# Kernel optimization log

Hardware: AMD Instinct MI355X
Metric: run time of the kernel (lower is better)

Reference implementation:

```python
import jax, jax.numpy as jnp
import numpy as np

N_NODES = 50000
N_EDGES = 800000
IN_DIM = 128
HIDDEN_DIMS = [128, 128]
OUT_DIM = 4
NUM_GRAPHS = 128


def setup_inputs() -> dict:
    key = jax.random.key(0)
    ks = jax.random.split(key, 12)
    inp = {
        "x": jax.random.normal(ks[0], (N_NODES, IN_DIM), dtype=jnp.float32),
        "edge_index": jax.random.randint(ks[1], (2, N_EDGES), 0, N_NODES, dtype=jnp.int64),
        "edge_attr": jax.random.uniform(ks[2], (N_EDGES,), dtype=jnp.float32),
        "edge_weight": jax.random.uniform(ks[3], (N_EDGES,), dtype=jnp.float32),
        "batch": jnp.sort(jax.random.randint(ks[4], (N_NODES,), 0, NUM_GRAPHS, dtype=jnp.int64)),
    }
    # GCNConv weights (Glorot-ish scale) and biases
    d_in = IN_DIM
    for i, d_out in enumerate(HIDDEN_DIMS):
        inp[f"W{i}"] = jax.random.normal(ks[5 + i], (d_in, d_out), dtype=jnp.float32) / np.sqrt(d_in)
        inp[f"b{i}"] = jnp.zeros((d_out,), dtype=jnp.float32)
        d_in = d_out
    # classifier: Linear(d,d) -> ReLU -> Linear(d,4)
    inp["Wc1"] = jax.random.normal(ks[8], (d_in, d_in), dtype=jnp.float32) / np.sqrt(d_in)
    inp["bc1"] = jnp.zeros((d_in,), dtype=jnp.float32)
    inp["Wc2"] = jax.random.normal(ks[9], (d_in, OUT_DIM), dtype=jnp.float32) / np.sqrt(d_in)
    inp["bc2"] = jnp.zeros((OUT_DIM,), dtype=jnp.float32)
    return inp


def _gcn_conv(x, src, dst, ew, W, b):
    # PyG GCNConv with add_self_loops=True, symmetric normalization.
    n = x.shape[0]
    loop = jnp.arange(n, dtype=src.dtype)
    s = jnp.concatenate([src, loop])
    d = jnp.concatenate([dst, loop])
    w = jnp.concatenate([ew, jnp.ones((n,), dtype=ew.dtype)])
    deg = jax.ops.segment_sum(w, d, num_segments=n)
    dinv = jnp.where(deg > 0, jax.lax.rsqrt(jnp.maximum(deg, 1e-12)), 0.0)
    norm = dinv[s] * w * dinv[d]  # [E+N]
    h = x @ W                     # [N, d_out] dense GEMM
    out = jax.ops.segment_sum(h[s] * norm[:, None], d, num_segments=n)
    return out + b


def reference(x, edge_index, edge_attr, edge_weight, batch,
              W0, b0, W1, b1, Wc1, bc1, Wc2, bc2):
    # NOTE: original code passes edge_attr into GCNConv's edge_weight slot;
    # edge_weight is unused. Dropout is identity (eval mode).
    src, dst = edge_index[0], edge_index[1]
    h = x
    for W, b in ((W0, b0), (W1, b1)):
        h = _gcn_conv(h, src, dst, edge_attr, W, b)
        h = jax.nn.relu(h)
    # global mean pool over graphs
    sums = jax.ops.segment_sum(h, batch, num_segments=NUM_GRAPHS)
    cnts = jax.ops.segment_sum(jnp.ones((h.shape[0],), h.dtype), batch, num_segments=NUM_GRAPHS)
    g = sums / jnp.maximum(cnts, 1.0)[:, None]  # [G, d]
    # classifier MLP
    g = jax.nn.relu(g @ Wc1 + bc1)
    return g @ Wc2 + bc2  # [G, 4]
```

## Files before the change

kernel.cpp:

```cpp
#include <hip/hip_runtime.h>
#include <hip/hip_fp16.h>

#define N_NODES 50000
#define N_EDGES 800000
#define DIM 128
#define NUM_GRAPHS 128
#define STRIDE 64
#define PSLICE 6272

#define ATTR_SCALE 33554432.0f
#define ATTR_MASK  ((1ull << 40) - 1)

typedef _Float16 f16x8 __attribute__((ext_vector_type(8)));
typedef float f32x4 __attribute__((ext_vector_type(4)));


__device__ __forceinline__ int pidx(int d) {
    return (d & 7) * PSLICE + (d >> 3);
}


__global__ __launch_bounds__(256) void k_build(const int* __restrict__ src,
                                               const int* __restrict__ dst,
                                               const float* __restrict__ attr,
                                               const float* __restrict__ W0,
                                               const float* __restrict__ W1,
                                               unsigned long long* packed,
                                               unsigned int* __restrict__ epack,
                                               _Float16* __restrict__ Wt0,
                                               _Float16* __restrict__ Wt1,
                                               int E, int nbChunks) {
    int b = blockIdx.x;
    if (b >= nbChunks * 8) {
        int idx = (b - nbChunks * 8) * 256 + threadIdx.x;
        int m = idx >> 14;
        int rem = idx & 16383;
        int n = rem >> 7;
        int k = rem & 127;
        const float* W = m ? W1 : W0;
        _Float16* Wt = m ? Wt1 : Wt0;
        Wt[(size_t)n * 128 + k] = (_Float16)W[(size_t)k * 128 + n];
        return;
    }
    int slice = b & 7;
    int e = (b >> 3) * 256 + threadIdx.x;
    if (e >= E) return;
    int d = dst[e];
    if ((d & 7) != slice) return;
    float a = attr[e];
    unsigned long long add =
        (1ull << 40) | (unsigned long long)(unsigned int)(a * ATTR_SCALE + 0.5f);
    unsigned long long old = atomicAdd(&packed[pidx(d)], add);
    int rank = (int)(old >> 40);
    if (rank < STRIDE) {
        __half ha = __float2half_rn(a);
        unsigned short us = *reinterpret_cast<unsigned short*>(&ha);
        epack[d * STRIDE + rank] = ((unsigned int)us << 16) | (unsigned int)src[e];
    }
}


template <typename AT>
__global__ __launch_bounds__(256) void k_gemm_mfma(const AT* __restrict__ A,
                                                   const _Float16* __restrict__ Wt,
                                                   const unsigned long long* __restrict__ packed,
                                                   __half* __restrict__ H, int n) {
    int tid = threadIdx.x;
    int w = tid >> 6, lane = tid & 63;
    int n15 = lane & 15, quad = lane >> 4;
    int node = blockIdx.x * 64 + w * 16 + n15;
    int nodec = node < n ? node : n - 1;
    const AT* Arow = A + (size_t)nodec * DIM;

    f32x4 acc[8];
#pragma unroll
    for (int t = 0; t < 8; t++) acc[t] = (f32x4){0.f, 0.f, 0.f, 0.f};

#pragma unroll
    for (int c = 0; c < 4; c++) {
        f16x8 bf;
        if constexpr (__is_same(AT, float)) {
            float4 a0 = ((const float4*)Arow)[c * 8 + quad * 2];
            float4 a1 = ((const float4*)Arow)[c * 8 + quad * 2 + 1];
            bf[0] = (_Float16)a0.x; bf[1] = (_Float16)a0.y;
            bf[2] = (_Float16)a0.z; bf[3] = (_Float16)a0.w;
            bf[4] = (_Float16)a1.x; bf[5] = (_Float16)a1.y;
            bf[6] = (_Float16)a1.z; bf[7] = (_Float16)a1.w;
        } else {
            const uint2* Ab = reinterpret_cast<const uint2*>(A);
            bf = *(const f16x8*)&Ab[((size_t)c * n + nodec) * 8 + quad * 2];
        }
#pragma unroll
        for (int t = 0; t < 8; t++) {
            f16x8 af = *(const f16x8*)(Wt + (size_t)(t * 16 + n15) * 128 + c * 32 + quad * 8);
            acc[t] = __builtin_amdgcn_mfma_f32_16x16x32_f16(af, bf, acc[t], 0, 0, 0);
        }
    }

    if (node < n) {
        unsigned long long pk = packed[pidx(nodec)];
        float dv = rsqrtf(1.0f + (float)(pk & ATTR_MASK) * (1.0f / ATTR_SCALE));
        uint2* Hb = (uint2*)H;
#pragma unroll
        for (int t = 0; t < 8; t++) {
            __half2 h01 = __floats2half2_rn(acc[t][0] * dv, acc[t][1] * dv);
            __half2 h23 = __floats2half2_rn(acc[t][2] * dv, acc[t][3] * dv);
            uint2 pkd;
            pkd.x = *reinterpret_cast<unsigned int*>(&h01);
            pkd.y = *reinterpret_cast<unsigned int*>(&h23);
            int colq = quad + 4 * t;
            Hb[((size_t)(colq >> 3) * n + node) * 8 + (colq & 7)] = pkd;
        }
    }
}


__device__ __forceinline__ float2 unpack_h2(unsigned int u) {
    __half2 h = *reinterpret_cast<__half2*>(&u);
    return __half22float2(h);
}

template <bool POOL>
__global__ __launch_bounds__(256) void k_gather(const __half* __restrict__ H,
                                                const unsigned long long* __restrict__ packed,
                                                const unsigned int* __restrict__ epack,
                                                const float* __restrict__ bias,
                                                const int* __restrict__ batch,
                                                __half* __restrict__ OUT,
                                                float* gsum, float* cnt, int n) {
    int cg = blockIdx.x & 3;
    int nb = blockIdx.x >> 2;
    int tid = threadIdx.x;

    __shared__ uint2 elds[STRIDE * 32];
    __shared__ float dv_lds[32];
    __shared__ int   cr_lds[32];

    {
        int slot = tid & 31;
        int kb = tid >> 5;
        int i1 = nb * 32 + slot;
        int ic1 = (i1 < n) ? i1 : n - 1;
        unsigned long long pk = packed[pidx(ic1)];
        int ce = (i1 < n) ? (int)(pk >> 40) : 0;
        if (ce > STRIDE) ce = STRIDE;
        int cr = (ce + 7) & ~7;
        if (kb == 0) {
            cr_lds[slot] = cr;
            dv_lds[slot] = rsqrtf(1.0f + (float)(pk & ATTR_MASK) * (1.0f / ATTR_SCALE));
        }
        const unsigned int* ep = epack + ic1 * STRIDE;
        for (int k = kb; k < cr; k += 8) {
            unsigned int pe = (k < ce) ? ep[k] : 0u;
            __half_raw hr;
            hr.x = (unsigned short)(pe >> 16);
            float wv = __half2float(__half(hr));
            elds[k * 32 + slot] = make_uint2((pe & 0xffffu) * 8u, __float_as_uint(wv));
        }
    }
    __syncthreads();

    int slot = tid >> 3;
    int ln = tid & 7;
    int i = nb * 32 + slot;
    bool valid = i < n;
    int ic = valid ? i : n - 1;
    int colq = cg * 8 + ln;
    const uint2* Hp = (const uint2*)H + (size_t)cg * n * 8;

    float dv = dv_lds[slot];
    int cr = cr_lds[slot];

    uint2 selfraw = Hp[(size_t)ic * 8 + ln];
    float2 s01 = unpack_h2(selfraw.x);
    float2 s23 = unpack_h2(selfraw.y);
    float4 acc = make_float4(s01.x, s01.y, s23.x, s23.y);

    for (int j = 0; j < cr; j += 8) {
        uint2 e[8];
#pragma unroll
        for (int k = 0; k < 8; k++) e[k] = elds[(j + k) * 32 + slot];
        uint2 v[8];
#pragma unroll
        for (int k = 0; k < 8; k++) v[k] = Hp[e[k].x + ln];
#pragma unroll
        for (int k = 0; k < 8; k++) {
            float wt = __uint_as_float(e[k].y);
            float2 f01 = unpack_h2(v[k].x);
            float2 f23 = unpack_h2(v[k].y);
            acc.x += wt * f01.x;
            acc.y += wt * f01.y;
            acc.z += wt * f23.x;
            acc.w += wt * f23.y;
        }
    }

    float4 bb = ((const float4*)bias)[colq];
    acc.x = fmaxf(acc.x * dv + bb.x, 0.f);
    acc.y = fmaxf(acc.y * dv + bb.y, 0.f);
    acc.z = fmaxf(acc.z * dv + bb.z, 0.f);
    acc.w = fmaxf(acc.w * dv + bb.w, 0.f);

    if constexpr (POOL) {
        __shared__ float lpool[32 * 32];
        __shared__ int sg[32];
        __shared__ int meta[4];
        if (ln == 0) sg[slot] = valid ? batch[ic] : -1;
        __syncthreads();
        if (tid == 0) {
            int nv = n - nb * 32; if (nv > 32) nv = 32;
            int gA = sg[0];
            int gB = sg[nv - 1];
            int cA = 0, cB = 0;
            for (int k2 = 0; k2 < nv; k2++) {
                if (sg[k2] == gA) cA++;
                else if (sg[k2] == gB) cB++;
            }
            meta[0] = gA; meta[1] = gB; meta[2] = cA; meta[3] = cB;
        }
        __syncthreads();
        int gA = meta[0], gB = meta[1];
        int myg = valid ? sg[slot] : -2;

        bool inA = valid && (myg == gA);
        ((float4*)(lpool + slot * 32))[ln] =
            inA ? acc : make_float4(0.f, 0.f, 0.f, 0.f);
        __syncthreads();
        if (tid < 32) {
            float ssum = 0.f;
#pragma unroll
            for (int k2 = 0; k2 < 32; k2++) ssum += lpool[k2 * 32 + tid];
            atomicAdd(&gsum[gA * DIM + cg * 32 + tid], ssum);
        }
        if (tid == 0 && cg == 0) atomicAdd(&cnt[gA], (float)meta[2]);

        if (gB != gA) {
            __syncthreads();
            bool inB = valid && (myg == gB);
            ((float4*)(lpool + slot * 32))[ln] =
                inB ? acc : make_float4(0.f, 0.f, 0.f, 0.f);
            __syncthreads();
            if (tid < 32) {
                float ssum = 0.f;
#pragma unroll
                for (int k2 = 0; k2 < 32; k2++) ssum += lpool[k2 * 32 + tid];
                atomicAdd(&gsum[gB * DIM + cg * 32 + tid], ssum);
            }
            if (tid == 0 && cg == 0) atomicAdd(&cnt[gB], (float)meta[3]);
        }

        if (valid && myg != gA && myg != gB) {
            float* o = gsum + (size_t)myg * DIM + cg * 32 + ln * 4;
            atomicAdd(o + 0, acc.x);
            atomicAdd(o + 1, acc.y);
            atomicAdd(o + 2, acc.z);
            atomicAdd(o + 3, acc.w);
            if (ln == 0 && cg == 0) atomicAdd(&cnt[myg], 1.0f);
        }
    } else {
        if (valid) {
            __half2 p01 = __floats2half2_rn(acc.x, acc.y);
            __half2 p23 = __floats2half2_rn(acc.z, acc.w);
            uint2 o;
            o.x = *reinterpret_cast<unsigned int*>(&p01);
            o.y = *reinterpret_cast<unsigned int*>(&p23);
            ((uint2*)OUT)[((size_t)cg * n + i) * 8 + ln] = o;
        }
    }
}


__global__ __launch_bounds__(128) void k_classifier(const float* __restrict__ gsum,
                                                    const float* __restrict__ cnt,
                                                    const float* __restrict__ Wc1,
                                                    const float* __restrict__ bc1,
                                                    const float* __restrict__ Wc2,
                                                    const float* __restrict__ bc2,
                                                    float* __restrict__ out) {
    int g = blockIdx.x;
    int t = threadIdx.x;
    __shared__ float gv[128];
    __shared__ float hid[128];
    float inv = 1.0f / fmaxf(cnt[g], 1.0f);
    gv[t] = gsum[(size_t)g * DIM + t] * inv;
    __syncthreads();
    float acc = bc1[t];
    for (int k = 0; k < 128; k++) acc += gv[k] * Wc1[k * 128 + t];
    hid[t] = fmaxf(acc, 0.f);
    __syncthreads();
    if (t < 4) {
        float o = bc2[t];
        for (int k = 0; k < 128; k++) o += hid[k] * Wc2[k * 4 + t];
        out[g * 4 + t] = o;
    }
}


extern "C" void kernel_launch(void* const* d_in, const int* in_sizes, int n_in,
                              void* d_out, int out_size, void* d_ws, size_t ws_size,
                              hipStream_t stream) {
    const float* x     = (const float*)d_in[0];
    const int*   ei    = (const int*)d_in[1];
    const float* attr  = (const float*)d_in[2];
    const int*   batch = (const int*)d_in[4];
    const float* W0  = (const float*)d_in[5];
    const float* b0  = (const float*)d_in[6];
    const float* W1  = (const float*)d_in[7];
    const float* b1  = (const float*)d_in[8];
    const float* Wc1 = (const float*)d_in[9];
    const float* bc1 = (const float*)d_in[10];
    const float* Wc2 = (const float*)d_in[11];
    const float* bc2 = (const float*)d_in[12];
    float* out = (float*)d_out;

    char* ws = (char*)d_ws;
    __half*             bufH16 = (__half*)(ws + 0);
    __half*             bufA16 = (__half*)(ws + 12800000);
    unsigned int*       epack  = (unsigned int*)(ws + 25600000);
    unsigned long long* packed = (unsigned long long*)(ws + 38400000);
    float*              gsum   = (float*)(ws + 38801408);
    float*              cnt    = (float*)(ws + 38866944);
    _Float16*           Wt0    = (_Float16*)(ws + 38867456);
    _Float16*           Wt1    = (_Float16*)(ws + 38900224);

    const int* src = ei;
    const int* dst = ei + N_EDGES;

    const int NB_C = (N_EDGES + 255) / 256;
    const int NB_G = ((N_NODES + 31) / 32) * 4;
    const int NB_M = (N_NODES + 63) / 64;

    (void)hipMemsetAsync(ws + 38400000, 0, 467456, stream);

    k_build<<<NB_C * 8 + 128, 256, 0, stream>>>(src, dst, attr, W0, W1, packed,
                                                epack, Wt0, Wt1, N_EDGES, NB_C);

    k_gemm_mfma<float><<<NB_M, 256, 0, stream>>>(x, Wt0, packed, bufH16, N_NODES);
    k_gather<false><<<NB_G, 256, 0, stream>>>(bufH16, packed, epack, b0,
                                              batch, bufA16, gsum, cnt, N_NODES);

    k_gemm_mfma<_Float16><<<NB_M, 256, 0, stream>>>((const _Float16*)bufA16, Wt1,
                                                    packed, bufH16, N_NODES);
    k_gather<true><<<NB_G, 256, 0, stream>>>(bufH16, packed, epack, b1,
                                             batch, nullptr, gsum, cnt, N_NODES);

    k_classifier<<<NUM_GRAPHS, 128, 0, stream>>>(gsum, cnt, Wc1, bc1, Wc2, bc2, out);
}
```

Baseline: 257.6 us.

## Fuse first-layer GEMM into build kernel and apply source degree scaling in gather

Runs the first-layer x@W0 GEMM inside the edge-build kernel, so it no longer has to wait for the degree accumulation; each block transposes W0 into LDS itself. Because degrees are not yet known at GEMM time, the source-side dinv scaling moves into the first gather via a new dinv array produced by a small extra kernel. The goal is to remove one launch and overlap the GEMM with the atomic-heavy edge bucketing. The cost is an extra kernel, a per-edge dinv lookup in gather staging, and every GEMM block redundantly converting W0.

```diff
diff --git a/kernel.cpp b/kernel.cpp
--- a/kernel.cpp
+++ b/kernel.cpp
@@ -20,30 +20,84 @@
 }
 
 
-__global__ __launch_bounds__(256) void k_build(const int* __restrict__ src,
+__global__ __launch_bounds__(256) void k_build(const float* __restrict__ x,
+                                               const int* __restrict__ src,
                                                const int* __restrict__ dst,
                                                const float* __restrict__ attr,
                                                const float* __restrict__ W0,
                                                const float* __restrict__ W1,
                                                unsigned long long* packed,
                                                unsigned int* __restrict__ epack,
-                                               _Float16* __restrict__ Wt0,
                                                _Float16* __restrict__ Wt1,
-                                               int E, int nbChunks) {
+                                               __half* __restrict__ H,
+                                               int E, int nbChunks, int nbGemm, int n) {
+    __shared__ _Float16 WtL[128 * 40];
     int b = blockIdx.x;
-    if (b >= nbChunks * 8) {
-        int idx = (b - nbChunks * 8) * 256 + threadIdx.x;
-        int m = idx >> 14;
-        int rem = idx & 16383;
-        int n = rem >> 7;
-        int k = rem & 127;
-        const float* W = m ? W1 : W0;
-        _Float16* Wt = m ? Wt1 : Wt0;
-        Wt[(size_t)n * 128 + k] = (_Float16)W[(size_t)k * 128 + n];
+    int tid = threadIdx.x;
+
+    if (b < nbGemm) {
+        int w = tid >> 6, lane = tid & 63;
+        int n15 = lane & 15, quad = lane >> 4;
+        int node = b * 64 + w * 16 + n15;
+        int nodec = node < n ? node : n - 1;
+        const float* Arow = x + (size_t)nodec * DIM;
+
+        f32x4 acc[8];
+#pragma unroll
+        for (int t = 0; t < 8; t++) acc[t] = (f32x4){0.f, 0.f, 0.f, 0.f};
+
+        for (int c = 0; c < 4; c++) {
+            __syncthreads();
+            {
+                int sn = tid & 127, kh = tid >> 7;
+#pragma unroll
+                for (int it = 0; it < 16; it++) {
+                    int kk = kh + it * 2;
+                    WtL[sn * 40 + kk] = (_Float16)W0[(size_t)(c * 32 + kk) * 128 + sn];
+                }
+            }
+            __syncthreads();
+            f16x8 bf;
+            float4 a0 = ((const float4*)Arow)[c * 8 + quad * 2];
+            float4 a1 = ((const float4*)Arow)[c * 8 + quad * 2 + 1];
+            bf[0] = (_Float16)a0.x; bf[1] = (_Float16)a0.y;
+            bf[2] = (_Float16)a0.z; bf[3] = (_Float16)a0.w;
+            bf[4] = (_Float16)a1.x; bf[5] = (_Float16)a1.y;
+            bf[6] = (_Float16)a1.z; bf[7] = (_Float16)a1.w;
+#pragma unroll
+            for (int t = 0; t < 8; t++) {
+                f16x8 af = *(const f16x8*)(WtL + (t * 16 + n15) * 40 + quad * 8);
+                acc[t] = __builtin_amdgcn_mfma_f32_16x16x32_f16(af, bf, acc[t], 0, 0, 0);
+            }
+        }
+
+        if (node < n) {
+            uint2* Hb = (uint2*)H;
+#pragma unroll
+            for (int t = 0; t < 8; t++) {
+                __half2 h01 = __floats2half2_rn(acc[t][0], acc[t][1]);
+                __half2 h23 = __floats2half2_rn(acc[t][2], acc[t][3]);
+                uint2 pkd;
+                pkd.x = *reinterpret_cast<unsigned int*>(&h01);
+                pkd.y = *reinterpret_cast<unsigned int*>(&h23);
+                int colq = quad + 4 * t;
+                Hb[((size_t)(colq >> 3) * n + node) * 8 + (colq & 7)] = pkd;
+            }
+        }
         return;
     }
-    int slice = b & 7;
-    int e = (b >> 3) * 256 + threadIdx.x;
+
+    if (b >= nbGemm + nbChunks * 8) {
+        int idx = (b - nbGemm - nbChunks * 8) * 256 + tid;
+        int nn = idx >> 7;
+        int kk = idx & 127;
+        Wt1[(size_t)nn * 128 + kk] = (_Float16)W1[(size_t)kk * 128 + nn];
+        return;
+    }
+
+    int b2 = b - nbGemm;
+    int slice = b2 & 7;
+    int e = (b2 >> 3) * 256 + tid;
     if (e >= E) return;
     int d = dst[e];
     if ((d & 7) != slice) return;
@@ -60,6 +114,16 @@
 }
 
 
+__global__ __launch_bounds__(256) void k_dinv(const unsigned long long* __restrict__ packed,
+                                              float* __restrict__ dinv, int n) {
+    int i = blockIdx.x * 256 + threadIdx.x;
+    if (i < n) {
+        unsigned long long pk = packed[pidx(i)];
+        dinv[i] = rsqrtf(1.0f + (float)(pk & ATTR_MASK) * (1.0f / ATTR_SCALE));
+    }
+}
+
+
 template <typename AT>
 __global__ __launch_bounds__(256) void k_gemm_mfma(const AT* __restrict__ A,
                                                    const _Float16* __restrict__ Wt,
@@ -120,10 +184,11 @@
     return __half22float2(h);
 }
 
-template <bool POOL>
+template <bool POOL, bool SRCS>
 __global__ __launch_bounds__(256) void k_gather(const __half* __restrict__ H,
                                                 const unsigned long long* __restrict__ packed,
                                                 const unsigned int* __restrict__ epack,
+                                                const float* __restrict__ dinv_arr,
                                                 const float* __restrict__ bias,
                                                 const int* __restrict__ batch,
                                                 __half* __restrict__ OUT,
@@ -155,6 +220,7 @@
             __half_raw hr;
             hr.x = (unsigned short)(pe >> 16);
             float wv = __half2float(__half(hr));
+            if (SRCS) wv *= dinv_arr[pe & 0xffffu];
             elds[k * 32 + slot] = make_uint2((pe & 0xffffu) * 8u, __float_as_uint(wv));
         }
     }
@@ -175,6 +241,9 @@
     float2 s01 = unpack_h2(selfraw.x);
     float2 s23 = unpack_h2(selfraw.y);
     float4 acc = make_float4(s01.x, s01.y, s23.x, s23.y);
+    if (SRCS) {
+        acc.x *= dv; acc.y *= dv; acc.z *= dv; acc.w *= dv;
+    }
 
     for (int j = 0; j < cr; j += 8) {
         uint2 e[8];
@@ -320,8 +389,8 @@
     unsigned long long* packed = (unsigned long long*)(ws + 38400000);
     float*              gsum   = (float*)(ws + 38801408);
     float*              cnt    = (float*)(ws + 38866944);
-    _Float16*           Wt0    = (_Float16*)(ws + 38867456);
-    _Float16*           Wt1    = (_Float16*)(ws + 38900224);
+    _Float16*           Wt1    = (_Float16*)(ws + 38867456);
+    float*              dinv   = (float*)(ws + 38900224);
 
     const int* src = ei;
     const int* dst = ei + N_EDGES;
@@ -329,20 +398,25 @@
     const int NB_C = (N_EDGES + 255) / 256;
     const int NB_G = ((N_NODES + 31) / 32) * 4;
     const int NB_M = (N_NODES + 63) / 64;
+    const int NB_D = (N_NODES + 255) / 256;
 
     (void)hipMemsetAsync(ws + 38400000, 0, 467456, stream);
 
-    k_build<<<NB_C * 8 + 128, 256, 0, stream>>>(src, dst, attr, W0, W1, packed,
-                                                epack, Wt0, Wt1, N_EDGES, NB_C);
-
-    k_gemm_mfma<float><<<NB_M, 256, 0, stream>>>(x, Wt0, packed, bufH16, N_NODES);
-    k_gather<false><<<NB_G, 256, 0, stream>>>(bufH16, packed, epack, b0,
-                                              batch, bufA16, gsum, cnt, N_NODES);
+    k_build<<<NB_M + NB_C * 8 + 64, 256, 0, stream>>>(x, src, dst, attr, W0, W1,
+                                                      packed, epack, Wt1, bufH16,
+                                                      N_EDGES, NB_C, NB_M, N_NODES);
+
+    k_dinv<<<NB_D, 256, 0, stream>>>(packed, dinv, N_NODES);
+
+    k_gather<false, true><<<NB_G, 256, 0, stream>>>(bufH16, packed, epack, dinv,
+                                                    b0, batch, bufA16, gsum, cnt,
+                                                    N_NODES);
 
     k_gemm_mfma<_Float16><<<NB_M, 256, 0, stream>>>((const _Float16*)bufA16, Wt1,
                                                     packed, bufH16, N_NODES);
-    k_gather<true><<<NB_G, 256, 0, stream>>>(bufH16, packed, epack, b1,
-                                             batch, nullptr, gsum, cnt, N_NODES);
+    k_gather<true, false><<<NB_G, 256, 0, stream>>>(bufH16, packed, epack, dinv,
+                                                    b1, batch, nullptr, gsum, cnt,
+                                                    N_NODES);
 
     k_classifier<<<NUM_GRAPHS, 128, 0, stream>>>(gsum, cnt, Wc1, bc1, Wc2, bc2, out);
 }
```

Measured after the change: 254.9 us. Within noise of the previous version (-1.1%).
